# Performance work log

Measured on AMD Instinct MI355X. Metric: run time of the kernel, lower is better.

Reference implementation:

```python
import jax, jax.numpy as jnp
import numpy as np

V, BS, E, H, L, FC = 50257, 1024, 768, 12, 6, 4
B, T = 4, 1024
HS = E // H
FF = FC * E
EPS = 1e-5


def setup_inputs() -> dict:
    key = jax.random.key(0)
    ks = jax.random.split(key, 24)
    s = 0.02
    inp = {
        'idx': jax.random.randint(ks[0], (B, T), 0, V),
        'targets': jax.random.randint(ks[1], (B, T), 0, V),
        'tok_emb': jax.random.normal(ks[2], (V, E), jnp.float32) * s,
        'pos_emb': jax.random.normal(ks[3], (BS, E), jnp.float32) * s,
        'Wq': jax.random.normal(ks[4], (L, H, E, HS), jnp.float32) * s,
        'Wk': jax.random.normal(ks[5], (L, H, E, HS), jnp.float32) * s,
        'Wv': jax.random.normal(ks[6], (L, H, E, HS), jnp.float32) * s,
        'Wo': jax.random.normal(ks[7], (L, E, E), jnp.float32) * s,
        'bo': jnp.zeros((L, E), jnp.float32),
        'ln1_s': jnp.ones((L, E), jnp.float32),
        'ln1_b': jnp.zeros((L, E), jnp.float32),
        'ln2_s': jnp.ones((L, E), jnp.float32),
        'ln2_b': jnp.zeros((L, E), jnp.float32),
        'W1': jax.random.normal(ks[8], (L, E, FF), jnp.float32) * s,
        'b1': jnp.zeros((L, FF), jnp.float32),
        'W2': jax.random.normal(ks[9], (L, FF, E), jnp.float32) * s,
        'b2': jnp.zeros((L, E), jnp.float32),
        'lnf_s': jnp.ones((E,), jnp.float32),
        'lnf_b': jnp.zeros((E,), jnp.float32),
        'Wlm': jax.random.normal(ks[10], (E, V), jnp.float32) * s,
        'blm': jnp.zeros((V,), jnp.float32),
    }
    return inp


def _ln(x, scale, bias):
    mu = x.mean(-1, keepdims=True)
    var = ((x - mu) ** 2).mean(-1, keepdims=True)
    return (x - mu) * jax.lax.rsqrt(var + EPS) * scale + bias


def _forward(idx, targets, tok_emb, pos_emb, Wq, Wk, Wv, Wo, bo,
             ln1_s, ln1_b, ln2_s, ln2_b, W1, b1, W2, b2,
             lnf_s, lnf_b, Wlm, blm):
    Bc, Tc = idx.shape
    x = tok_emb[idx] + pos_emb[:Tc]                      # [B,T,E]
    causal = jnp.tril(jnp.ones((Tc, Tc), bool))          # [T,T]

    def block(x, p):
        wq, wk, wv, wo_, bo_, l1s, l1b, l2s, l2b, w1, b1_, w2, b2_ = p
        h = _ln(x, l1s, l1b)
        q = jnp.einsum('bte,hed->bhtd', h, wq)
        k = jnp.einsum('bte,hed->bhtd', h, wk)
        v = jnp.einsum('bte,hed->bhtd', h, wv)
        scores = jnp.einsum('bhtd,bhsd->bhts', q, k) * (HS ** -0.5)
        scores = jnp.where(causal, scores, -jnp.inf)
        att = jax.nn.softmax(scores, axis=-1)            # [B,H,T,T]
        o = jnp.einsum('bhts,bhsd->bhtd', att, v)
        o = o.transpose(0, 2, 1, 3).reshape(Bc, Tc, E)   # concat heads
        x = x + jnp.einsum('bte,ef->btf', o, wo_) + bo_
        h2 = _ln(x, l2s, l2b)
        f = jax.nn.relu(jnp.einsum('bte,ef->btf', h2, w1) + b1_)
        x = x + jnp.einsum('btf,fe->bte', f, w2) + b2_
        return x, None

    layers = (Wq, Wk, Wv, Wo, bo, ln1_s, ln1_b, ln2_s, ln2_b, W1, b1, W2, b2)
    x, _ = jax.lax.scan(block, x, layers)
    x = _ln(x, lnf_s, lnf_b)
    logits = jnp.einsum('bte,ev->btv', x, Wlm) + blm     # [B,T,V]
    logp = jax.nn.log_softmax(logits, axis=-1)
    nll = -jnp.take_along_axis(logp, targets[..., None], axis=-1)[..., 0]
    loss = nll.mean()
    return logits, loss


def reference(idx, targets, tok_emb, pos_emb, Wq, Wk, Wv, Wo, bo,
              ln1_s, ln1_b, ln2_s, ln2_b, W1, b1, W2, b2,
              lnf_s, lnf_b, Wlm, blm):
    return _forward(idx, targets, tok_emb, pos_emb, Wq, Wk, Wv, Wo, bo,
                    ln1_s, ln1_b, ln2_s, ln2_b, W1, b1, W2, b2,
                    lnf_s, lnf_b, Wlm, blm)
```

## Files before the change

kernel.cpp:

```cpp
#include <hip/hip_runtime.h>
#include <hip/hip_bf16.h>
#include <cstdint>
#include <cstddef>

#define NB 4
#define NT 1024
#define NE 768
#define NH 12
#define NHS 64
#define NL 6
#define NFF 3072
#define NV 50257
#define NVP 50304
#define NTOK (NB*NT)
#define NCB_LM (NVP/128)
#define QKVS 2304

typedef __attribute__((ext_vector_type(8))) short short8;
typedef __attribute__((ext_vector_type(4))) float f32x4;
typedef __hip_bfloat16 bf16;

__global__ __launch_bounds__(256) void embed_kernel(
    const int* __restrict__ idx, const float* __restrict__ tok,
    const float* __restrict__ pos, float* __restrict__ x)
{
  int bt = blockIdx.x;
  int token = idx[bt];
  int t = bt & (NT - 1);
  const float* tr = tok + (size_t)token * NE;
  const float* pr = pos + (size_t)t * NE;
  float* xr = x + (size_t)bt * NE;
  for (int i = threadIdx.x; i < NE; i += 256)
    xr[i] = tr[i] + pr[i];
}

__global__ __launch_bounds__(256) void ln_kernel(
    const float* __restrict__ in, const float* __restrict__ sc,
    const float* __restrict__ bi, bf16* __restrict__ out)
{
  int row = blockIdx.x, tid = threadIdx.x;
  const float* xr = in + (size_t)row * NE;
  float v0 = xr[tid], v1 = xr[tid + 256], v2 = xr[tid + 512];
  float s = v0 + v1 + v2;
  float ss = v0 * v0 + v1 * v1 + v2 * v2;
  #pragma unroll
  for (int o = 32; o > 0; o >>= 1) {
    s  += __shfl_xor(s, o);
    ss += __shfl_xor(ss, o);
  }
  __shared__ float r1[4], r2[4];
  if ((tid & 63) == 0) { r1[tid >> 6] = s; r2[tid >> 6] = ss; }
  __syncthreads();
  float tot = r1[0] + r1[1] + r1[2] + r1[3];
  float tss = r2[0] + r2[1] + r2[2] + r2[3];
  float mu  = tot * (1.f / NE);
  float var = tss * (1.f / NE) - mu * mu;
  float rs  = rsqrtf(var + 1e-5f);
  bf16* orow = out + (size_t)row * NE;
  orow[tid]       = __float2bfloat16((v0 - mu) * rs * sc[tid]       + bi[tid]);
  orow[tid + 256] = __float2bfloat16((v1 - mu) * rs * sc[tid + 256] + bi[tid + 256]);
  orow[tid + 512] = __float2bfloat16((v2 - mu) * rs * sc[tid + 512] + bi[tid + 512]);
}

__global__ __launch_bounds__(256) void tconv_kernel(
    const float* __restrict__ src, bf16* __restrict__ dst,
    int R, int Cs, int Cd, int zdiv,
    size_t srcZstr, size_t dstLstr, size_t dstHstr)
{
  __shared__ float t[32][33];
  int z = blockIdx.z;
  int l = z / zdiv, h = z - l * zdiv;
  src += (size_t)z * srcZstr;
  dst += (size_t)l * dstLstr + (size_t)h * dstHstr;
  int c0 = blockIdx.x * 32, r0 = blockIdx.y * 32;
  int tx = threadIdx.x & 31, ty = threadIdx.x >> 5;
  #pragma unroll
  for (int i = 0; i < 32; i += 8) {
    int r = r0 + ty + i, c = c0 + tx;
    t[ty + i][tx] = (c < Cs) ? src[(size_t)r * Cs + c] : 0.f;
  }
  __syncthreads();
  #pragma unroll
  for (int i = 0; i < 32; i += 8) {
    int c = c0 + ty + i, r = r0 + tx;
    if (c < Cd) dst[(size_t)c * R + r] = __float2bfloat16(t[tx][ty + i]);
  }
}

template<int MREP, bool SWZ>
__global__ __launch_bounds__(256) void gemm_bf(
    const bf16* __restrict__ A,
    const bf16* __restrict__ BT,
    float* __restrict__ Cf, bf16* __restrict__ Cbf,
    const float* __restrict__ bias, const float* __restrict__ Rres,
    float* __restrict__ ps,
    int M, int N, int K, int relu, int ncb)
{
  constexpr int BMT = MREP * 32;
  __shared__ bf16 As[BMT][64];
  __shared__ bf16 Bs[128][64];
  __shared__ float ps2[BMT][2];
  int tid = threadIdx.x;
  int lane = tid & 63;
  int w = __builtin_amdgcn_readfirstlane(tid >> 6);
  int wr = w >> 1, wc = w & 1;
  int cb = blockIdx.x;
  int row0 = blockIdx.y * BMT;
  int col0 = cb * 128;

  f32x4 acc[MREP][4] = {};

  for (int k0 = 0; k0 < K; k0 += 64) {
    #pragma unroll
    for (int r = 0; r < MREP; ++r) {
      int c = r * 256 + tid;
      int trow = c >> 3;
      int schunk = SWZ ? ((c & 7) ^ (trow & 7)) : (c & 7);
      const bf16* ga = A + (size_t)(row0 + trow) * K + k0 + (schunk << 3);
      __builtin_amdgcn_global_load_lds(
          (const __attribute__((address_space(1))) void*)ga,
          (__attribute__((address_space(3))) void*)((char*)&As[0][0] + (unsigned)c * 16),
          16, 0, 0);
    }
    #pragma unroll
    for (int r = 0; r < 4; ++r) {
      int c = r * 256 + tid;
      int trow = c >> 3;
      int schunk = SWZ ? ((c & 7) ^ (trow & 7)) : (c & 7);
      const bf16* gb = BT + (size_t)(col0 + trow) * K + k0 + (schunk << 3);
      __builtin_amdgcn_global_load_lds(
          (const __attribute__((address_space(1))) void*)gb,
          (__attribute__((address_space(3))) void*)((char*)&Bs[0][0] + (unsigned)c * 16),
          16, 0, 0);
    }
    __syncthreads();
    int l15 = lane & 15;
    int g8 = (lane >> 4) << 3;
    int sx = SWZ ? ((l15 & 7) << 3) : 0;
    #pragma unroll
    for (int kk = 0; kk < 64; kk += 32) {
      short8 a[MREP], b[4];
      #pragma unroll
      for (int m = 0; m < MREP; ++m)
        a[m] = *(const short8*)&As[wr * (MREP * 16) + m * 16 + l15][(kk + g8) ^ sx];
      #pragma unroll
      for (int n = 0; n < 4; ++n)
        b[n] = *(const short8*)&Bs[wc * 64 + n * 16 + l15][(kk + g8) ^ sx];
      #pragma unroll
      for (int m = 0; m < MREP; ++m)
        #pragma unroll
        for (int n = 0; n < 4; ++n)
          acc[m][n] = __builtin_amdgcn_mfma_f32_16x16x32_bf16(a[m], b[n], acc[m][n], 0, 0, 0);
    }
    __syncthreads();
  }

  int cr = lane >> 4;
  int cc = lane & 15;
  #pragma unroll
  for (int m = 0; m < MREP; ++m) {
    #pragma unroll
    for (int n = 0; n < 4; ++n) {
      int col = col0 + wc * 64 + n * 16 + cc;
      if (col >= N) continue;
      float bv = bias ? bias[col] : 0.f;
      #pragma unroll
      for (int e = 0; e < 4; ++e) {
        int row = row0 + wr * (MREP * 16) + m * 16 + cr * 4 + e;
        float v = acc[m][n][e] + bv;
        size_t off = (size_t)row * N + col;
        if (Rres) v += Rres[off];
        if (relu) v = fmaxf(v, 0.f);
        if (Cf)  Cf[off] = v;
        if (Cbf) Cbf[off] = __float2bfloat16(v);
      }
    }
  }

  if (ps) {
    #pragma unroll
    for (int m = 0; m < MREP; ++m) {
      #pragma unroll
      for (int e = 0; e < 4; ++e) {
        float ssum = 0.f;
        #pragma unroll
        for (int n = 0; n < 4; ++n) {
          int col = col0 + wc * 64 + n * 16 + cc;
          float val = (col < N) ? (acc[m][n][e] + (bias ? bias[col] : 0.f)) : -1e30f;
          ssum += __expf(val);
        }
        ssum += __shfl_xor(ssum, 1);
        ssum += __shfl_xor(ssum, 2);
        ssum += __shfl_xor(ssum, 4);
        ssum += __shfl_xor(ssum, 8);
        if (cc == 0) {
          int rl = wr * (MREP * 16) + m * 16 + cr * 4 + e;
          ps2[rl][wc] = ssum;
        }
      }
    }
    __syncthreads();
    for (int i = tid; i < MREP * 32; i += 256) {
      size_t o = (size_t)(row0 + i) * ncb + cb;
      ps[o] = ps2[i][0] + ps2[i][1];
    }
  }
}

#define LBK 32
#define LMK 768
__global__ __launch_bounds__(256) void lm_gemm(
    const bf16* __restrict__ A, const bf16* __restrict__ BT,
    float* __restrict__ Cf, const float* __restrict__ bias,
    float* __restrict__ ps, int M, int N, int ncb)
{
  __shared__ bf16 As[2][128][LBK];
  __shared__ bf16 Bs[2][128][LBK];
  float (*ps2)[2] = reinterpret_cast<float(*)[2]>(&As[0][0][0]);
  int tid = threadIdx.x;
  int lane = tid & 63;
  int w = __builtin_amdgcn_readfirstlane(tid >> 6);
  int wr = w >> 1, wc = w & 1;
  int row0 = blockIdx.y * 128, col0 = blockIdx.x * 128;
  int l15 = lane & 15;
  int g8 = (lane >> 4) << 3;

  f32x4 acc[4][4] = {};
  const int nk = LMK / LBK;

#define LM_STAGE(b, k0)                                                        \
  {                                                                            \
    _Pragma("unroll")                                                          \
    for (int r = 0; r < 2; ++r) {                                              \
      int c = r * 256 + tid;                                                   \
      int trow = c >> 2, tcol = (c & 3) << 3;                                  \
      const bf16* ga = A + (size_t)(row0 + trow) * LMK + (k0) + tcol;          \
      __builtin_amdgcn_global_load_lds(                                        \
          (const __attribute__((address_space(1))) void*)ga,                   \
          (__attribute__((address_space(3))) void*)((char*)&As[b][0][0] + (unsigned)c * 16), \
          16, 0, 0);                                                           \
    }                                                                          \
    _Pragma("unroll")                                                          \
    for (int r = 0; r < 2; ++r) {                                              \
      int c = r * 256 + tid;                                                   \
      int trow = c >> 2, tcol = (c & 3) << 3;                                  \
      const bf16* gb = BT + (size_t)(col0 + trow) * LMK + (k0) + tcol;         \
      __builtin_amdgcn_global_load_lds(                                        \
          (const __attribute__((address_space(1))) void*)gb,                   \
          (__attribute__((address_space(3))) void*)((char*)&Bs[b][0][0] + (unsigned)c * 16), \
          16, 0, 0);                                                           \
    }                                                                          \
  }

  LM_STAGE(0, 0);
  asm volatile("s_waitcnt vmcnt(0)" ::: "memory");
  __builtin_amdgcn_s_barrier();

  int cur = 0;
  for (int t = 0; t < nk - 1; ++t) {
    LM_STAGE(cur ^ 1, (t + 1) * LBK);
    short8 a[4], bb[4];
    #pragma unroll
    for (int m = 0; m < 4; ++m)
      a[m] = *(const short8*)&As[cur][wr * 64 + m * 16 + l15][g8];
    #pragma unroll
    for (int n = 0; n < 4; ++n)
      bb[n] = *(const short8*)&Bs[cur][wc * 64 + n * 16 + l15][g8];
    #pragma unroll
    for (int m = 0; m < 4; ++m)
      #pragma unroll
      for (int n = 0; n < 4; ++n)
        acc[m][n] = __builtin_amdgcn_mfma_f32_16x16x32_bf16(a[m], bb[n], acc[m][n], 0, 0, 0);
    asm volatile("s_waitcnt vmcnt(0)" ::: "memory");
    __builtin_amdgcn_s_barrier();
    cur ^= 1;
  }
  {
    short8 a[4], bb[4];
    #pragma unroll
    for (int m = 0; m < 4; ++m)
      a[m] = *(const short8*)&As[cur][wr * 64 + m * 16 + l15][g8];
    #pragma unroll
    for (int n = 0; n < 4; ++n)
      bb[n] = *(const short8*)&Bs[cur][wc * 64 + n * 16 + l15][g8];
    #pragma unroll
    for (int m = 0; m < 4; ++m)
      #pragma unroll
      for (int n = 0; n < 4; ++n)
        acc[m][n] = __builtin_amdgcn_mfma_f32_16x16x32_bf16(a[m], bb[n], acc[m][n], 0, 0, 0);
  }

  int cr = lane >> 4;
  int cc = lane & 15;
  #pragma unroll
  for (int m = 0; m < 4; ++m) {
    #pragma unroll
    for (int n = 0; n < 4; ++n) {
      int col = col0 + wc * 64 + n * 16 + cc;
      if (col >= N) continue;
      float bv = bias[col];
      #pragma unroll
      for (int e = 0; e < 4; ++e) {
        int row = row0 + wr * 64 + m * 16 + cr * 4 + e;
        Cf[(size_t)row * N + col] = acc[m][n][e] + bv;
      }
    }
  }

  #pragma unroll
  for (int m = 0; m < 4; ++m) {
    #pragma unroll
    for (int e = 0; e < 4; ++e) {
      float ssum = 0.f;
      #pragma unroll
      for (int n = 0; n < 4; ++n) {
        int col = col0 + wc * 64 + n * 16 + cc;
        float val = (col < N) ? (acc[m][n][e] + bias[col]) : -1e30f;
        ssum += __expf(val);
      }
      ssum += __shfl_xor(ssum, 1);
      ssum += __shfl_xor(ssum, 2);
      ssum += __shfl_xor(ssum, 4);
      ssum += __shfl_xor(ssum, 8);
      if (cc == 0) ps2[wr * 64 + m * 16 + cr * 4 + e][wc] = ssum;
    }
  }
  __syncthreads();
  for (int i = tid; i < 128; i += 256) {
    size_t o = (size_t)(row0 + i) * ncb + blockIdx.x;
    ps[o] = ps2[i][0] + ps2[i][1];
  }
#undef LM_STAGE
}

static __device__ inline unsigned short bfbits(float x) {
  bf16 h = __float2bfloat16(x);
  return *reinterpret_cast<unsigned short*>(&h);
}

__global__ __launch_bounds__(256) void fattn_kernel(
    const bf16* __restrict__ QKV, bf16* __restrict__ O)
{
  __shared__ unsigned short Ks[64][72];
  __shared__ unsigned short Vt[64][72];
  __shared__ unsigned short Pl[4][16][72];
  int qt = blockIdx.x, h = blockIdx.y, b = blockIdx.z;
  int tid = threadIdx.x;
  int lane = tid & 63;
  int w = tid >> 6;
  int l15 = lane & 15, g = lane >> 4;
  int brow = b * NT;
  int qbase = qt * 64;
  int q_loc = w * 16 + l15;

  short8 bq[2];
  {
    const bf16* qp = QKV + (size_t)(brow + qbase + q_loc) * QKVS + h * 64 + g * 8;
    bq[0] = *(const short8*)qp;
    bq[1] = *(const short8*)(qp + 32);
  }

  short8 kreg[2], vreg[2];
  int c0t = tid, c1t = tid + 256;
  int row0t = c0t >> 3, colg0 = (c0t & 7) * 8;
  int row1t = c1t >> 3, colg1 = (c1t & 7) * 8;

  auto LOADKV = [&](int kt) {
    int s0 = kt * 64;
    const bf16* base0 = QKV + (size_t)(brow + s0 + row0t) * QKVS + h * 64;
    const bf16* base1 = QKV + (size_t)(brow + s0 + row1t) * QKVS + h * 64;
    kreg[0] = *(const short8*)(base0 + NE + colg0);
    vreg[0] = *(const short8*)(base0 + 2 * NE + colg0);
    kreg[1] = *(const short8*)(base1 + NE + colg1);
    vreg[1] = *(const short8*)(base1 + 2 * NE + colg1);
  };

  float m_run = -1e30f, l_run = 0.f;
  f32x4 acc[4] = {};

  LOADKV(0);
  for (int kt = 0; kt <= qt; ++kt) {
    *(short8*)&Ks[row0t][colg0] = kreg[0];
    *(short8*)&Ks[row1t][colg1] = kreg[1];
    #pragma unroll
    for (int j = 0; j < 8; ++j) {
      Vt[colg0 + j][row0t] = (unsigned short)vreg[0][j];
      Vt[colg1 + j][row1t] = (unsigned short)vreg[1][j];
    }
    __syncthreads();
    if (kt < qt) LOADKV(kt + 1);

    f32x4 sf[4] = {};
    #pragma unroll
    for (int kk = 0; kk < 2; ++kk) {
      #pragma unroll
      for (int m = 0; m < 4; ++m) {
        short8 a = *(const short8*)&Ks[m * 16 + l15][kk * 32 + g * 8];
        sf[m] = __builtin_amdgcn_mfma_f32_16x16x32_bf16(a, bq[kk], sf[m], 0, 0, 0);
      }
    }

    float sv[4][4];
    float mx = -1e30f;
    bool diag = (kt == qt);
    #pragma unroll
    for (int m = 0; m < 4; ++m)
      #pragma unroll
      for (int e = 0; e < 4; ++e) {
        float v = sf[m][e] * 0.125f;
        if (diag) {
          int sl = m * 16 + g * 4 + e;
          if (sl > q_loc) v = -1e30f;
        }
        sv[m][e] = v;
        mx = fmaxf(mx, v);
      }
    mx = fmaxf(mx, __shfl_xor(mx, 16));
    mx = fmaxf(mx, __shfl_xor(mx, 32));

    if (!__all(mx - m_run <= 8.f)) {
      float m_new = fmaxf(m_run, mx);
      float sc_old = __expf(m_run - m_new);
      l_run *= sc_old;
      #pragma unroll
      for (int dm = 0; dm < 4; ++dm)
        #pragma unroll
        for (int e = 0; e < 4; ++e)
          acc[dm][e] *= sc_old;
      m_run = m_new;
    }

    float p[4][4];
    float rs = 0.f;
    #pragma unroll
    for (int m = 0; m < 4; ++m)
      #pragma unroll
      for (int e = 0; e < 4; ++e) {
        float pe = __expf(sv[m][e] - m_run);
        p[m][e] = pe;
        rs += pe;
      }
    rs += __shfl_xor(rs, 16);
    rs += __shfl_xor(rs, 32);
    l_run += rs;

    #pragma unroll
    for (int m = 0; m < 4; ++m)
      #pragma unroll
      for (int ep = 0; ep < 2; ++ep) {
        unsigned u = (unsigned)bfbits(p[m][2 * ep]) |
                     ((unsigned)bfbits(p[m][2 * ep + 1]) << 16);
        *(unsigned*)&Pl[w][l15][m * 16 + g * 4 + ep * 2] = u;
      }

    #pragma unroll
    for (int ks = 0; ks < 2; ++ks) {
      short8 pb = *(const short8*)&Pl[w][l15][ks * 32 + g * 8];
      #pragma unroll
      for (int dm = 0; dm < 4; ++dm) {
        short8 av = *(const short8*)&Vt[dm * 16 + l15][ks * 32 + g * 8];
        acc[dm] = __builtin_amdgcn_mfma_f32_16x16x32_bf16(av, pb, acc[dm], 0, 0, 0);
      }
    }
    __syncthreads();
  }

  float inv = 1.f / l_run;
  bf16* op = O + (size_t)(brow + qbase + q_loc) * NE + h * 64;
  #pragma unroll
  for (int dm = 0; dm < 4; ++dm)
    #pragma unroll
    for (int ep = 0; ep < 2; ++ep) {
      int d = dm * 16 + g * 4 + ep * 2;
      unsigned u = (unsigned)bfbits(acc[dm][2 * ep] * inv) |
                   ((unsigned)bfbits(acc[dm][2 * ep + 1] * inv) << 16);
      *(unsigned*)((unsigned short*)op + d) = u;
    }
}

__global__ __launch_bounds__(128) void nll_finish(
    const float* __restrict__ ps,
    const float* __restrict__ logits, const int* __restrict__ targets,
    float* __restrict__ nll)
{
  int row = blockIdx.x, tid = threadIdx.x;
  float s = 0.f;
  for (int i = tid; i < NCB_LM; i += 128)
    s += ps[(size_t)row * NCB_LM + i];
  #pragma unroll
  for (int o = 32; o > 0; o >>= 1) s += __shfl_xor(s, o);
  __shared__ float ss[2];
  if ((tid & 63) == 0) ss[tid >> 6] = s;
  __syncthreads();
  if (tid == 0) {
    float S = ss[0] + ss[1];
    float tgt = logits[(size_t)row * NV + targets[row]];
    nll[row] = logf(S) - tgt;
  }
}

__global__ __launch_bounds__(256) void loss_kernel(
    const float* __restrict__ nll, float* __restrict__ out)
{
  int tid = threadIdx.x;
  float s = 0.f;
  for (int i = tid; i < NTOK; i += 256) s += nll[i];
  #pragma unroll
  for (int o = 32; o > 0; o >>= 1) s += __shfl_xor(s, o);
  __shared__ float red[4];
  if ((tid & 63) == 0) red[tid >> 6] = s;
  __syncthreads();
  if (tid == 0) out[0] = (red[0] + red[1] + red[2] + red[3]) * (1.f / NTOK);
}

static inline void gemm(const bf16* A, const bf16* BT,
                        float* Cf, bf16* Cbf,
                        const float* bias, const float* Rres, float* ps,
                        int M, int N, int Npad, int K, int relu,
                        int mrep, hipStream_t st)
{
  int ncb = Npad / 128;
  dim3 g(ncb, M / (mrep * 32));
  if (mrep == 4)
    gemm_bf<4, true><<<g, dim3(256), 0, st>>>(A, BT, Cf, Cbf, bias, Rres, ps, M, N, K, relu, ncb);
  else
    gemm_bf<2, true><<<g, dim3(256), 0, st>>>(A, BT, Cf, Cbf, bias, Rres, ps, M, N, K, relu, ncb);
}

extern "C" void kernel_launch(void* const* d_in, const int* in_sizes, int n_in,
                              void* d_out, int out_size, void* d_ws, size_t ws_size,
                              hipStream_t stream)
{
  const int*   idx     = (const int*)  d_in[0];
  const int*   targets = (const int*)  d_in[1];
  const float* tok_emb = (const float*)d_in[2];
  const float* pos_emb = (const float*)d_in[3];
  const float* Wq      = (const float*)d_in[4];
  const float* Wk      = (const float*)d_in[5];
  const float* Wv      = (const float*)d_in[6];
  const float* Wo      = (const float*)d_in[7];
  const float* bo      = (const float*)d_in[8];
  const float* ln1_s   = (const float*)d_in[9];
  const float* ln1_b   = (const float*)d_in[10];
  const float* ln2_s   = (const float*)d_in[11];
  const float* ln2_b   = (const float*)d_in[12];
  const float* W1      = (const float*)d_in[13];
  const float* b1      = (const float*)d_in[14];
  const float* W2      = (const float*)d_in[15];
  const float* b2      = (const float*)d_in[16];
  const float* lnf_s   = (const float*)d_in[17];
  const float* lnf_b   = (const float*)d_in[18];
  const float* Wlm     = (const float*)d_in[19];
  const float* blm     = (const float*)d_in[20];
  float* out = (float*)d_out;

  const size_t XE = (size_t)NTOK * NE;
  char* p = (char*)d_ws;
  float* x     = (float*)p;         p += XE * 4;
  bf16* h_bf   = (bf16*)p;          p += XE * 2;
  bf16* qkv_bf = (bf16*)p;          p += (size_t)NTOK * QKVS * 2;
  bf16* att_bf = (bf16*)p;          p += XE * 2;
  bf16* f_bf   = (bf16*)p;          p += (size_t)NTOK * NFF * 2;
  bf16* wqkv_a = (bf16*)p;          p += (size_t)NL * QKVS * NE * 2;
  bf16* wto_a  = (bf16*)p;          p += (size_t)NL * NE * NE * 2;
  bf16* wt1_a  = (bf16*)p;          p += (size_t)NL * NFF * NE * 2;
  bf16* wt2_a  = (bf16*)p;          p += (size_t)NL * NE * NFF * 2;
  bf16* wtlm   = (bf16*)p;          p += (size_t)NVP * NE * 2;
  float* psb   = (float*)p;         p += (size_t)NTOK * NCB_LM * 4;
  float* nll   = (float*)p;         p += (size_t)NTOK * 4;

  embed_kernel<<<dim3(NTOK), dim3(256), 0, stream>>>(idx, tok_emb, pos_emb, x);

  tconv_kernel<<<dim3(2, 24, NL * NH), dim3(256), 0, stream>>>(
      Wq, wqkv_a, NE, NHS, NHS, NH,
      (size_t)NE * NHS, (size_t)QKVS * NE, (size_t)NHS * NE);
  tconv_kernel<<<dim3(2, 24, NL * NH), dim3(256), 0, stream>>>(
      Wk, wqkv_a + (size_t)NE * NE, NE, NHS, NHS, NH,
      (size_t)NE * NHS, (size_t)QKVS * NE, (size_t)NHS * NE);
  tconv_kernel<<<dim3(2, 24, NL * NH), dim3(256), 0, stream>>>(
      Wv, wqkv_a + (size_t)2 * NE * NE, NE, NHS, NHS, NH,
      (size_t)NE * NHS, (size_t)QKVS * NE, (size_t)NHS * NE);
  tconv_kernel<<<dim3(24, 24, NL), dim3(256), 0, stream>>>(
      Wo, wto_a, NE, NE, NE, 1, (size_t)NE * NE, (size_t)NE * NE, 0);
  tconv_kernel<<<dim3(96, 24, NL), dim3(256), 0, stream>>>(
      W1, wt1_a, NE, NFF, NFF, 1, (size_t)NE * NFF, (size_t)NFF * NE, 0);
  tconv_kernel<<<dim3(24, 96, NL), dim3(256), 0, stream>>>(
      W2, wt2_a, NFF, NE, NE, 1, (size_t)NFF * NE, (size_t)NE * NFF, 0);

  for (int l = 0; l < NL; ++l) {
    ln_kernel<<<dim3(NTOK), dim3(256), 0, stream>>>(x, ln1_s + l*NE, ln1_b + l*NE, h_bf);

    gemm(h_bf, wqkv_a + (size_t)l * QKVS * NE, nullptr, qkv_bf, nullptr, nullptr, nullptr,
         NTOK, QKVS, QKVS, NE, 0, 4, stream);

    fattn_kernel<<<dim3(NT / 64, NH, NB), dim3(256), 0, stream>>>(qkv_bf, att_bf);

    gemm(att_bf, wto_a + (size_t)l * NE * NE, x, nullptr, bo + l*NE, x, nullptr,
         NTOK, NE, NE, NE, 0, 2, stream);

    ln_kernel<<<dim3(NTOK), dim3(256), 0, stream>>>(x, ln2_s + l*NE, ln2_b + l*NE, h_bf);

    gemm(h_bf, wt1_a + (size_t)l * NFF * NE, nullptr, f_bf, b1 + l*NFF, nullptr, nullptr,
         NTOK, NFF, NFF, NE, 1, 4, stream);
    gemm(f_bf, wt2_a + (size_t)l * NE * NFF, x, nullptr, b2 + l*NE, x, nullptr,
         NTOK, NE, NE, NFF, 0, 2, stream);
  }

  ln_kernel<<<dim3(NTOK), dim3(256), 0, stream>>>(x, lnf_s, lnf_b, h_bf);

  tconv_kernel<<<dim3(NVP / 32, 24, 1), dim3(256), 0, stream>>>(
      Wlm, wtlm, NE, NV, NVP, 1, 0, 0, 0);

  {
    dim3 g(NCB_LM, NTOK / 128);
    lm_gemm<<<g, dim3(256), 0, stream>>>(h_bf, wtlm, out, blm, psb,
                                         NTOK, NV, NCB_LM);
  }

  nll_finish<<<dim3(NTOK), dim3(128), 0, stream>>>(psb, out, targets, nll);
  loss_kernel<<<dim3(1), dim3(256), 0, stream>>>(nll, out + (size_t)NTOK * NV);
}
```

Baseline: 2.091 ms.

## Enlarge flash-attention query tile to 128 rows with 8 waves per block

The attention kernel now processes 128 query rows per block using 512 threads (8 waves), so each K/V tile staged in shared memory is reused by twice as many queries. Each thread loads one K/V chunk instead of two, and the causal mask is generalized to handle the two diagonal key tiles. This halves K/V global traffic and LDS staging per query. In exchange there are fewer blocks (384 instead of 768), more imbalanced causal work per block, and larger blocks that may lower occupancy.

```diff
diff --git a/kernel.cpp b/kernel.cpp
--- a/kernel.cpp
+++ b/kernel.cpp
@@ -338,19 +338,19 @@
   return *reinterpret_cast<unsigned short*>(&h);
 }
 
-__global__ __launch_bounds__(256) void fattn_kernel(
+__global__ __launch_bounds__(512) void fattn_kernel(
     const bf16* __restrict__ QKV, bf16* __restrict__ O)
 {
   __shared__ unsigned short Ks[64][72];
   __shared__ unsigned short Vt[64][72];
-  __shared__ unsigned short Pl[4][16][72];
+  __shared__ unsigned short Pl[8][16][72];
   int qt = blockIdx.x, h = blockIdx.y, b = blockIdx.z;
   int tid = threadIdx.x;
   int lane = tid & 63;
   int w = tid >> 6;
   int l15 = lane & 15, g = lane >> 4;
   int brow = b * NT;
-  int qbase = qt * 64;
+  int qbase = qt * 128;
   int q_loc = w * 16 + l15;
 
   short8 bq[2];
@@ -360,35 +360,28 @@
     bq[1] = *(const short8*)(qp + 32);
   }
 
-  short8 kreg[2], vreg[2];
-  int c0t = tid, c1t = tid + 256;
-  int row0t = c0t >> 3, colg0 = (c0t & 7) * 8;
-  int row1t = c1t >> 3, colg1 = (c1t & 7) * 8;
+  short8 kreg, vreg;
+  int rowt = tid >> 3, colgt = (tid & 7) * 8;
 
   auto LOADKV = [&](int kt) {
     int s0 = kt * 64;
-    const bf16* base0 = QKV + (size_t)(brow + s0 + row0t) * QKVS + h * 64;
-    const bf16* base1 = QKV + (size_t)(brow + s0 + row1t) * QKVS + h * 64;
-    kreg[0] = *(const short8*)(base0 + NE + colg0);
-    vreg[0] = *(const short8*)(base0 + 2 * NE + colg0);
-    kreg[1] = *(const short8*)(base1 + NE + colg1);
-    vreg[1] = *(const short8*)(base1 + 2 * NE + colg1);
+    const bf16* base = QKV + (size_t)(brow + s0 + rowt) * QKVS + h * 64;
+    kreg = *(const short8*)(base + NE + colgt);
+    vreg = *(const short8*)(base + 2 * NE + colgt);
   };
 
   float m_run = -1e30f, l_run = 0.f;
   f32x4 acc[4] = {};
+  const int nkt = 2 * qt + 2;
 
   LOADKV(0);
-  for (int kt = 0; kt <= qt; ++kt) {
-    *(short8*)&Ks[row0t][colg0] = kreg[0];
-    *(short8*)&Ks[row1t][colg1] = kreg[1];
-    #pragma unroll
-    for (int j = 0; j < 8; ++j) {
-      Vt[colg0 + j][row0t] = (unsigned short)vreg[0][j];
-      Vt[colg1 + j][row1t] = (unsigned short)vreg[1][j];
-    }
+  for (int kt = 0; kt < nkt; ++kt) {
+    *(short8*)&Ks[rowt][colgt] = kreg;
+    #pragma unroll
+    for (int j = 0; j < 8; ++j)
+      Vt[colgt + j][rowt] = (unsigned short)vreg[j];
     __syncthreads();
-    if (kt < qt) LOADKV(kt + 1);
+    if (kt + 1 < nkt) LOADKV(kt + 1);
 
     f32x4 sf[4] = {};
     #pragma unroll
@@ -402,14 +395,15 @@
 
     float sv[4][4];
     float mx = -1e30f;
-    bool diag = (kt == qt);
+    bool diag = (kt >= 2 * qt);
+    int sbase = kt * 64 - qbase;
     #pragma unroll
     for (int m = 0; m < 4; ++m)
       #pragma unroll
       for (int e = 0; e < 4; ++e) {
         float v = sf[m][e] * 0.125f;
         if (diag) {
-          int sl = m * 16 + g * 4 + e;
+          int sl = sbase + m * 16 + g * 4 + e;
           if (sl > q_loc) v = -1e30f;
         }
         sv[m][e] = v;
@@ -593,7 +587,7 @@
     gemm(h_bf, wqkv_a + (size_t)l * QKVS * NE, nullptr, qkv_bf, nullptr, nullptr, nullptr,
          NTOK, QKVS, QKVS, NE, 0, 4, stream);
 
-    fattn_kernel<<<dim3(NT / 64, NH, NB), dim3(256), 0, stream>>>(qkv_bf, att_bf);
+    fattn_kernel<<<dim3(NT / 128, NH, NB), dim3(512), 0, stream>>>(qkv_bf, att_bf);
 
     gemm(att_bf, wto_a + (size_t)l * NE * NE, x, nullptr, bo + l*NE, x, nullptr,
          NTOK, NE, NE, NE, 0, 2, stream);
```

Result: no change. 2.071 ms (-1.0%).
